# Kernel optimization log

Measured on AMD Instinct MI355X. Metric: run time of the kernel, lower is better.

Reference implementation:

```python
import jax, jax.numpy as jnp
import numpy as np

NUM_HEADS = 16  # concat repeats the identical head output this many times


def setup_inputs() -> dict:
    key = jax.random.key(0)
    ks = jax.random.split(key, 6)
    B, S, E, D = 4, 4096, 1024, 64  # D = E // NUM_HEADS
    s_in = 1.0 / np.sqrt(E)
    return {
        "x": jax.random.normal(ks[0], (B, S, E), dtype=jnp.float32),
        "Wq": jax.random.normal(ks[1], (E, D), dtype=jnp.float32) * s_in,
        "bq": jnp.zeros((D,), dtype=jnp.float32),
        "Wk": jax.random.normal(ks[2], (E, D), dtype=jnp.float32) * s_in,
        "bk": jnp.zeros((D,), dtype=jnp.float32),
        "Wv": jax.random.normal(ks[3], (E, D), dtype=jnp.float32) * s_in,
        "bv": jnp.zeros((D,), dtype=jnp.float32),
        "Wo": jax.random.normal(ks[4], (E, E), dtype=jnp.float32) * s_in,
        "bo": jnp.zeros((E,), dtype=jnp.float32),
    }


def reference(x, Wq, bq, Wk, bk, Wv, bv, Wo, bo):
    # Single shared projection to head_dim (the torch code projects E -> E//H once).
    q = x @ Wq + bq          # [B,S,D]
    k = x @ Wk + bk          # [B,S,D]
    v = x @ Wv + bv          # [B,S,D]
    d = q.shape[-1]
    scale = 1.0 / jnp.sqrt(jnp.asarray(d, dtype=q.dtype))
    scores = jnp.einsum("bqd,bkd->bqk", q, k) * scale   # [B,S,S]
    attn = jax.nn.softmax(scores, axis=-1)
    ctx = jnp.einsum("bqk,bkd->bqd", attn, v)            # [B,S,D]
    # Every head computes the identical result; concat == tile along features.
    cat = jnp.tile(ctx, (1, 1, NUM_HEADS))               # [B,S,E]
    return cat @ Wo + bo
```

## Files before the change

kernel.cpp:

```cpp
#include <hip/hip_runtime.h>
#include <hip/hip_bf16.h>

#define BB 4
#define SS 4096
#define EE 1024
#define DD 64

typedef unsigned short u16;
typedef unsigned int   u32;
typedef __bf16 bf16_t;
typedef bf16_t bf16x8 __attribute__((ext_vector_type(8)));
typedef float  f32x4  __attribute__((ext_vector_type(4)));
typedef u32    u32x4  __attribute__((ext_vector_type(4)));

__device__ __forceinline__ u16 f2bf(float f) {
    u32 u; __builtin_memcpy(&u, &f, 4);
    u32 r = (u + 0x7FFFu + ((u >> 16) & 1u)) >> 16;
    return (u16)r;
}
__device__ __forceinline__ u16 f2bf_fast(float f) {
    u32 u; __builtin_memcpy(&u, &f, 4);
    return (u16)((u + 0x8000u) >> 16);
}

__global__ __launch_bounds__(256) void wt_kernel(const float* __restrict__ Wq,
                                                 const float* __restrict__ Wk,
                                                 const float* __restrict__ Wv,
                                                 u16* __restrict__ Wt) {
    int t = blockIdx.x * 256 + threadIdx.x;
    int c = t >> 10, e = t & 1023;
    const float* W = (c < 64) ? Wq : (c < 128) ? Wk : Wv;
    Wt[c * 1024 + e] = f2bf(W[e * 64 + (c & 63)]);
}

__global__ __launch_bounds__(256) void wosum_kernel(const float* __restrict__ Wo,
                                                    float* __restrict__ WoSum) {
    int t = blockIdx.x * 256 + threadIdx.x;
    int d = t >> 10, e = t & 1023;
    float s = 0.f;
    #pragma unroll
    for (int h = 0; h < 16; h++) s += Wo[(h * 64 + d) * 1024 + e];
    WoSum[t] = s;
}

__global__ __launch_bounds__(256) void proj_kernel(const float* __restrict__ x,
                                                   const u16* __restrict__ Wtg,
                                                   const float* __restrict__ bq,
                                                   const float* __restrict__ bk,
                                                   const float* __restrict__ bv,
                                                   u16* __restrict__ Qg,
                                                   u16* __restrict__ Kg,
                                                   u16* __restrict__ Vtg) {
    __shared__ __align__(16) u16 xt[32 * 136];
    __shared__ __align__(16) u16 wts[192 * 136];

    const int tid  = threadIdx.x;
    const int w    = tid >> 6;
    const int lane = tid & 63;
    const int m    = lane & 15;
    const int quad = lane >> 4;
    const int r0   = blockIdx.x * 32;
    const int mt   = w & 1;
    const int ch   = w >> 1;

    f32x4 acc[6];
    #pragma unroll
    for (int i = 0; i < 6; i++) acc[i] = (f32x4){0.f, 0.f, 0.f, 0.f};

    f32x4 xr[4];
    u32x4 wr[12];

    auto preload = [&](int kb) {
        #pragma unroll
        for (int j = 0; j < 2; j++) {
            const int id = tid + j * 256, row = id >> 4, seg = id & 15;
            const float* src = x + (r0 + row) * 1024 + kb * 128 + seg * 8;
            xr[2 * j]     = *(const f32x4*)(src);
            xr[2 * j + 1] = *(const f32x4*)(src + 4);
        }
        #pragma unroll
        for (int j = 0; j < 12; j++) {
            const int id = tid + j * 256, row = id >> 4, seg = id & 15;
            wr[j] = *(const u32x4*)(Wtg + row * 1024 + kb * 128 + seg * 8);
        }
    };
    auto commit = [&]() {
        #pragma unroll
        for (int j = 0; j < 2; j++) {
            const int id = tid + j * 256, row = id >> 4, seg = id & 15;
            u32x4 p;
            p[0] = (u32)f2bf(xr[2*j][0])   | ((u32)f2bf(xr[2*j][1]) << 16);
            p[1] = (u32)f2bf(xr[2*j][2])   | ((u32)f2bf(xr[2*j][3]) << 16);
            p[2] = (u32)f2bf(xr[2*j+1][0]) | ((u32)f2bf(xr[2*j+1][1]) << 16);
            p[3] = (u32)f2bf(xr[2*j+1][2]) | ((u32)f2bf(xr[2*j+1][3]) << 16);
            *(u32x4*)(xt + row * 136 + seg * 8) = p;
        }
        #pragma unroll
        for (int j = 0; j < 12; j++) {
            const int id = tid + j * 256, row = id >> 4, seg = id & 15;
            *(u32x4*)(wts + row * 136 + seg * 8) = wr[j];
        }
    };

    preload(0);
    for (int kb = 0; kb < 8; kb++) {
        __syncthreads();
        commit();
        __syncthreads();
        if (kb < 7) preload(kb + 1);
        #pragma unroll
        for (int ks = 0; ks < 4; ks++) {
            bf16x8 a = *(const bf16x8*)(xt + (mt * 16 + m) * 136 + ks * 32 + quad * 8);
            #pragma unroll
            for (int c = 0; c < 6; c++) {
                bf16x8 b = *(const bf16x8*)(wts + (ch * 96 + c * 16 + m) * 136 + ks * 32 + quad * 8);
                acc[c] = __builtin_amdgcn_mfma_f32_16x16x32_bf16(a, b, acc[c], 0, 0, 0);
            }
        }
    }

    const int rbase = r0 + mt * 16 + quad * 4;
    #pragma unroll
    for (int c = 0; c < 6; c++) {
        const int col   = ch * 96 + c * 16 + m;
        const int which = col >> 6;
        const int d     = col & 63;
        const float bias = (which == 0 ? bq : which == 1 ? bk : bv)[d];
        #pragma unroll
        for (int r = 0; r < 4; r++) {
            const int row = rbase + r;
            float v = acc[c][r] + bias;
            if (which == 0) {
                Qg[row * 64 + d] = f2bf(v * 0.125f);
            } else if (which == 1) {
                Kg[row * 64 + d] = f2bf(v);
            } else {
                const int b = row >> 12, s = row & 4095;
                Vtg[(b * 64 + d) * 4096 + s] = f2bf(v);
            }
        }
    }
}

#define ATTN_LDS 147456
__global__ __launch_bounds__(512) void attn_kernel(const u16* __restrict__ Qg,
                                                   const u16* __restrict__ Kg,
                                                   const u16* __restrict__ Vtg,
                                                   float* __restrict__ ctxg) {
    extern __shared__ __align__(16) u16 smem[];

    const int tid  = threadIdx.x;
    const int w    = tid >> 6;
    const int lane = tid & 63;
    const int m    = lane & 15;
    const int quad = lane >> 4;

    const int bi    = blockIdx.x;
    const int batch = (bi >> 1) & 3;
    const int qt    = ((bi >> 3) << 1) | (bi & 1);
    const int qrow0 = batch * 4096 + qt * 64;

    u16* wbase = smem + w * 9216;

    bf16x8 aq[4][2];
    #pragma unroll
    for (int s = 0; s < 4; s++) {
        aq[s][0] = *(const bf16x8*)(Qg + (qrow0 + s * 16 + m) * 64 + quad * 8);
        aq[s][1] = *(const bf16x8*)(Qg + (qrow0 + s * 16 + m) * 64 + 32 + quad * 8);
    }

    f32x4 acc[4][4];
    float li[4][4];
    #pragma unroll
    for (int s = 0; s < 4; s++)
        #pragma unroll
        for (int c = 0; c < 4; c++) {
            acc[s][c] = (f32x4){0.f, 0.f, 0.f, 0.f};
            li[s][c] = 0.f;
        }

    const u16* Kbase = Kg + batch * 4096 * 64;
    const u16* Vbase = Vtg + batch * 64 * 4096;

    const int rl8 = lane >> 3, sg8 = lane & 7;
    const int rv  = lane >> 2, sv  = lane & 3;

    u32x4 kr[4], vr[4];
    auto preload = [&](int it) {
        const int k0 = (w + it * 8) * 32;
        #pragma unroll
        for (int i = 0; i < 4; i++) {
            kr[i] = *(const u32x4*)(Kbase + (k0 + rl8 + 8 * i) * 64 + sg8 * 8);
            vr[i] = *(const u32x4*)(Vbase + (rv + 16 * i) * 4096 + k0 + sv * 8);
        }
    };
    auto commitKV = [&](int p) {
        u16* Kt = wbase + p * 4608;
        u16* Vt = Kt + 2560;
        #pragma unroll
        for (int i = 0; i < 4; i++) {
            *(u32x4*)(Kt + (rl8 + 8 * i) * 64 + ((sg8 ^ rl8) * 8)) = kr[i];
            *(u32x4*)(Vt + (rv + 16 * i) * 32 + sv * 8) = vr[i];
        }
    };

    const float LOG2E = 1.4426950408889634f;
    const float NC2   = -12.0f * 1.4426950408889634f;

    preload(0);
    commitKV(0);

    for (int it = 0; it < 16; it++) {
        const int pcur = it & 1;
        u16* Kt = wbase + pcur * 4608;
        u16* Vt = Kt + 2560;
        u16* P  = Kt;

        if (it < 15) preload(it + 1);

        f32x4 sc[4][2];
        #pragma unroll
        for (int c = 0; c < 2; c++) {
            const int key = c * 16 + m;
            bf16x8 b0 = *(const bf16x8*)(Kt + key * 64 + ((quad ^ (m & 7)) * 8));
            bf16x8 b1 = *(const bf16x8*)(Kt + key * 64 + (((quad | 4) ^ (m & 7)) * 8));
            #pragma unroll
            for (int s = 0; s < 4; s++) {
                f32x4 t = __builtin_amdgcn_mfma_f32_16x16x32_bf16(aq[s][0], b0, (f32x4){0.f,0.f,0.f,0.f}, 0, 0, 0);
                sc[s][c] = __builtin_amdgcn_mfma_f32_16x16x32_bf16(aq[s][1], b1, t, 0, 0, 0);
            }
        }

        #pragma unroll
        for (int s = 0; s < 4; s++) {
            #pragma unroll
            for (int r = 0; r < 4; r++) {
                const float p0 = __builtin_exp2f(__builtin_fmaf(sc[s][0][r], LOG2E, NC2));
                const float p1 = __builtin_exp2f(__builtin_fmaf(sc[s][1][r], LOG2E, NC2));
                li[s][r] += p0 + p1;
                const int row = s * 16 + quad * 4 + r;
                P[row * 40 + m]      = f2bf_fast(p0);
                P[row * 40 + 16 + m] = f2bf_fast(p1);
            }
        }

        bf16x8 ap[4];
        #pragma unroll
        for (int s = 0; s < 4; s++)
            ap[s] = *(const bf16x8*)(P + (s * 16 + m) * 40 + quad * 8);
        #pragma unroll
        for (int c = 0; c < 4; c++) {
            bf16x8 bv = *(const bf16x8*)(Vt + (c * 16 + m) * 32 + quad * 8);
            #pragma unroll
            for (int s = 0; s < 4; s++)
                acc[s][c] = __builtin_amdgcn_mfma_f32_16x16x32_bf16(ap[s], bv, acc[s][c], 0, 0, 0);
        }

        if (it < 15) commitKV((it + 1) & 1);
    }

    #pragma unroll
    for (int s = 0; s < 4; s++)
        #pragma unroll
        for (int r = 0; r < 4; r++) {
            float v = li[s][r];
            v += __shfl_xor(v, 1);
            v += __shfl_xor(v, 2);
            v += __shfl_xor(v, 4);
            v += __shfl_xor(v, 8);
            li[s][r] = v;
        }

    __syncthreads();
    float* mf = (float*)smem;
    if (w >= 4) {
        float* cb = mf + (w - 4) * 4160;
        #pragma unroll
        for (int s = 0; s < 4; s++)
            #pragma unroll
            for (int c = 0; c < 4; c++)
                #pragma unroll
                for (int r = 0; r < 4; r++)
                    cb[(s * 16 + quad * 4 + r) * 64 + c * 16 + m] = acc[s][c][r];
        if (m == 0) {
            #pragma unroll
            for (int s = 0; s < 4; s++)
                #pragma unroll
                for (int r = 0; r < 4; r++)
                    cb[4096 + s * 16 + quad * 4 + r] = li[s][r];
        }
    }
    __syncthreads();
    if (w < 4) {
        float* cb = mf + w * 4160;
        #pragma unroll
        for (int s = 0; s < 4; s++)
            #pragma unroll
            for (int c = 0; c < 4; c++)
                #pragma unroll
                for (int r = 0; r < 4; r++)
                    acc[s][c][r] += cb[(s * 16 + quad * 4 + r) * 64 + c * 16 + m];
        #pragma unroll
        for (int s = 0; s < 4; s++)
            #pragma unroll
            for (int r = 0; r < 4; r++)
                li[s][r] += cb[4096 + s * 16 + quad * 4 + r];
        #pragma unroll
        for (int s = 0; s < 4; s++)
            #pragma unroll
            for (int c = 0; c < 4; c++)
                #pragma unroll
                for (int r = 0; r < 4; r++)
                    cb[(s * 16 + quad * 4 + r) * 64 + c * 16 + m] = acc[s][c][r];
        if (m == 0) {
            #pragma unroll
            for (int s = 0; s < 4; s++)
                #pragma unroll
                for (int r = 0; r < 4; r++)
                    cb[4096 + s * 16 + quad * 4 + r] = li[s][r];
        }
    }
    __syncthreads();

    const int q  = tid >> 3;
    const int d0 = (tid & 7) * 8;
    float L = 0.f;
    f32x4 o0 = (f32x4){0.f, 0.f, 0.f, 0.f};
    f32x4 o1 = (f32x4){0.f, 0.f, 0.f, 0.f};
    #pragma unroll
    for (int j = 0; j < 4; j++) {
        const float* cb = mf + j * 4160;
        L  += cb[4096 + q];
        o0 += *(const f32x4*)(cb + q * 64 + d0);
        o1 += *(const f32x4*)(cb + q * 64 + d0 + 4);
    }
    const float inv = 1.0f / L;
    o0 *= inv; o1 *= inv;
    *(f32x4*)(ctxg + (qrow0 + q) * 64 + d0)     = o0;
    *(f32x4*)(ctxg + (qrow0 + q) * 64 + d0 + 4) = o1;
}

__global__ __launch_bounds__(256) void out_kernel(const float* __restrict__ ctxg,
                                                  const float* __restrict__ WoSum,
                                                  const float* __restrict__ bo,
                                                  float* __restrict__ out) {
    __shared__ float cl[64 * 64];
    const int tid = threadIdx.x;
    const int r0  = (blockIdx.x >> 2) * 64;
    const int eb  = (blockIdx.x & 3) * 256;

    #pragma unroll
    for (int j = 0; j < 4; j++) {
        const int pos = (tid + j * 256) * 4;
        *(f32x4*)(cl + pos) = *(const f32x4*)(ctxg + r0 * 64 + pos);
    }
    __syncthreads();

    const int rg = tid >> 6;
    const int cg = tid & 63;
    const int e0 = eb + cg * 4;

    f32x4 bo4 = *(const f32x4*)(bo + e0);
    f32x4 a[16];
    #pragma unroll
    for (int r = 0; r < 16; r++) a[r] = bo4;

    for (int d = 0; d < 64; d++) {
        f32x4 wv = *(const f32x4*)(WoSum + d * 1024 + e0);
        #pragma unroll
        for (int r = 0; r < 16; r++) {
            a[r] += wv * cl[(rg * 16 + r) * 64 + d];
        }
    }
    #pragma unroll
    for (int r = 0; r < 16; r++) {
        *(f32x4*)(out + (r0 + rg * 16 + r) * 1024 + e0) = a[r];
    }
}

extern "C" void kernel_launch(void* const* d_in, const int* in_sizes, int n_in,
                              void* d_out, int out_size, void* d_ws, size_t ws_size,
                              hipStream_t stream) {
    const float* x  = (const float*)d_in[0];
    const float* Wq = (const float*)d_in[1];
    const float* bq = (const float*)d_in[2];
    const float* Wk = (const float*)d_in[3];
    const float* bk = (const float*)d_in[4];
    const float* Wv = (const float*)d_in[5];
    const float* bv = (const float*)d_in[6];
    const float* Wo = (const float*)d_in[7];
    const float* bo = (const float*)d_in[8];
    float* out = (float*)d_out;

    char* ws = (char*)d_ws;
    u16*   Wt   = (u16*)(ws);
    float* WoS  = (float*)(ws + 393216);
    u16*   Qg   = (u16*)(ws + 655360);
    u16*   Kg   = (u16*)(ws + 2752512);
    u16*   Vtg  = (u16*)(ws + 4849664);
    float* ctxg = (float*)(ws + 6946816);

    (void)hipFuncSetAttribute((const void*)attn_kernel,
                              hipFuncAttributeMaxDynamicSharedMemorySize, ATTN_LDS);

    wt_kernel   <<<768,  256, 0, stream>>>(Wq, Wk, Wv, Wt);
    wosum_kernel<<<256,  256, 0, stream>>>(Wo, WoS);
    proj_kernel <<<512,  256, 0, stream>>>(x, Wt, bq, bk, bv, Qg, Kg, Vtg);
    attn_kernel <<<256,  512, ATTN_LDS, stream>>>(Qg, Kg, Vtg, ctxg);
    out_kernel  <<<1024, 256, 0, stream>>>(ctxg, WoS, bo, out);
}
```

Before: 217.5 us.

## Split attention keys across two blocks, merge partials in output kernel

The attention kernel now splits each batch's keys into two halves handled by separate blocks, doubling the grid to 512 blocks. It drops the LDS double buffer to halve shared memory and adds a launch-bounds occupancy hint. Each block writes unnormalized partial context and row sums, and the output GEMM kernel adds the two halves and applies the 1/L normalization. The kernel also computes row sums with an MFMA against a ones vector instead of shuffles, uses hardware bf16 conversion and packed P stores with a permuted V layout, and pads the reduction scratch to cut bank conflicts. This is meant to raise occupancy and parallelism on the 256-CU device, at the cost of extra partial-result traffic and a single-buffered K/V pipeline.

```diff
diff --git a/kernel.cpp b/kernel.cpp
--- a/kernel.cpp
+++ b/kernel.cpp
@@ -9,18 +9,15 @@
 typedef unsigned short u16;
 typedef unsigned int   u32;
 typedef __bf16 bf16_t;
+typedef bf16_t bf16x2 __attribute__((ext_vector_type(2)));
 typedef bf16_t bf16x8 __attribute__((ext_vector_type(8)));
 typedef float  f32x4  __attribute__((ext_vector_type(4)));
 typedef u32    u32x4  __attribute__((ext_vector_type(4)));
 
-__device__ __forceinline__ u16 f2bf(float f) {
-    u32 u; __builtin_memcpy(&u, &f, 4);
-    u32 r = (u + 0x7FFFu + ((u >> 16) & 1u)) >> 16;
-    return (u16)r;
-}
-__device__ __forceinline__ u16 f2bf_fast(float f) {
-    u32 u; __builtin_memcpy(&u, &f, 4);
-    return (u16)((u + 0x8000u) >> 16);
+__device__ __forceinline__ u16 f2bf_hw(float f) {
+    bf16_t b = (bf16_t)f;
+    u16 u; __builtin_memcpy(&u, &b, 2);
+    return u;
 }
 
 __global__ __launch_bounds__(256) void wt_kernel(const float* __restrict__ Wq,
@@ -30,7 +27,7 @@
     int t = blockIdx.x * 256 + threadIdx.x;
     int c = t >> 10, e = t & 1023;
     const float* W = (c < 64) ? Wq : (c < 128) ? Wk : Wv;
-    Wt[c * 1024 + e] = f2bf(W[e * 64 + (c & 63)]);
+    Wt[c * 1024 + e] = f2bf_hw(W[e * 64 + (c & 63)]);
 }
 
 __global__ __launch_bounds__(256) void wosum_kernel(const float* __restrict__ Wo,
@@ -88,12 +85,13 @@
         #pragma unroll
         for (int j = 0; j < 2; j++) {
             const int id = tid + j * 256, row = id >> 4, seg = id & 15;
-            u32x4 p;
-            p[0] = (u32)f2bf(xr[2*j][0])   | ((u32)f2bf(xr[2*j][1]) << 16);
-            p[1] = (u32)f2bf(xr[2*j][2])   | ((u32)f2bf(xr[2*j][3]) << 16);
-            p[2] = (u32)f2bf(xr[2*j+1][0]) | ((u32)f2bf(xr[2*j+1][1]) << 16);
-            p[3] = (u32)f2bf(xr[2*j+1][2]) | ((u32)f2bf(xr[2*j+1][3]) << 16);
-            *(u32x4*)(xt + row * 136 + seg * 8) = p;
+            bf16x8 v;
+            #pragma unroll
+            for (int k = 0; k < 4; k++) {
+                v[k]     = (bf16_t)xr[2 * j][k];
+                v[4 + k] = (bf16_t)xr[2 * j + 1][k];
+            }
+            *(bf16x8*)(xt + row * 136 + seg * 8) = v;
         }
         #pragma unroll
         for (int j = 0; j < 12; j++) {
@@ -131,22 +129,24 @@
             const int row = rbase + r;
             float v = acc[c][r] + bias;
             if (which == 0) {
-                Qg[row * 64 + d] = f2bf(v * 0.125f);
+                Qg[row * 64 + d] = f2bf_hw(v * 0.125f);
             } else if (which == 1) {
-                Kg[row * 64 + d] = f2bf(v);
+                Kg[row * 64 + d] = f2bf_hw(v);
             } else {
                 const int b = row >> 12, s = row & 4095;
-                Vtg[(b * 64 + d) * 4096 + s] = f2bf(v);
+                const int sp = (s & ~31) | (((s & 15) << 1) | ((s >> 4) & 1));
+                Vtg[(b * 64 + d) * 4096 + sp] = f2bf_hw(v);
             }
         }
     }
 }
 
-#define ATTN_LDS 147456
-__global__ __launch_bounds__(512) void attn_kernel(const u16* __restrict__ Qg,
-                                                   const u16* __restrict__ Kg,
-                                                   const u16* __restrict__ Vtg,
-                                                   float* __restrict__ ctxg) {
+#define ATTN_LDS 73728
+__global__ __launch_bounds__(512, 4) void attn_kernel(const u16* __restrict__ Qg,
+                                                      const u16* __restrict__ Kg,
+                                                      const u16* __restrict__ Vtg,
+                                                      float* __restrict__ ctxP,
+                                                      float* __restrict__ liP) {
     extern __shared__ __align__(16) u16 smem[];
 
     const int tid  = threadIdx.x;
@@ -156,11 +156,14 @@
     const int quad = lane >> 4;
 
     const int bi    = blockIdx.x;
+    const int khalf = bi & 1;
     const int batch = (bi >> 1) & 3;
-    const int qt    = ((bi >> 3) << 1) | (bi & 1);
+    const int qt    = bi >> 3;
     const int qrow0 = batch * 4096 + qt * 64;
 
-    u16* wbase = smem + w * 9216;
+    u16* wbase = smem + w * 4608;
+    u16* Kt = wbase;
+    u16* Vt = wbase + 2560;
 
     bf16x8 aq[4][2];
     #pragma unroll
@@ -170,17 +173,20 @@
     }
 
     f32x4 acc[4][4];
-    float li[4][4];
-    #pragma unroll
-    for (int s = 0; s < 4; s++)
-        #pragma unroll
-        for (int c = 0; c < 4; c++) {
-            acc[s][c] = (f32x4){0.f, 0.f, 0.f, 0.f};
-            li[s][c] = 0.f;
-        }
-
-    const u16* Kbase = Kg + batch * 4096 * 64;
-    const u16* Vbase = Vtg + batch * 64 * 4096;
+    f32x4 accli[4];
+    #pragma unroll
+    for (int s = 0; s < 4; s++) {
+        accli[s] = (f32x4){0.f, 0.f, 0.f, 0.f};
+        #pragma unroll
+        for (int c = 0; c < 4; c++) acc[s][c] = (f32x4){0.f, 0.f, 0.f, 0.f};
+    }
+
+    bf16x8 ones;
+    #pragma unroll
+    for (int k = 0; k < 8; k++) ones[k] = (bf16_t)1.0f;
+
+    const u16* Kbase = Kg + (batch * 4096 + khalf * 2048) * 64;
+    const u16* Vbase = Vtg + batch * 64 * 4096 + khalf * 2048;
 
     const int rl8 = lane >> 3, sg8 = lane & 7;
     const int rv  = lane >> 2, sv  = lane & 3;
@@ -194,9 +200,7 @@
             vr[i] = *(const u32x4*)(Vbase + (rv + 16 * i) * 4096 + k0 + sv * 8);
         }
     };
-    auto commitKV = [&](int p) {
-        u16* Kt = wbase + p * 4608;
-        u16* Vt = Kt + 2560;
+    auto commitKV = [&]() {
         #pragma unroll
         for (int i = 0; i < 4; i++) {
             *(u32x4*)(Kt + (rl8 + 8 * i) * 64 + ((sg8 ^ rl8) * 8)) = kr[i];
@@ -208,15 +212,10 @@
     const float NC2   = -12.0f * 1.4426950408889634f;
 
     preload(0);
-    commitKV(0);
-
-    for (int it = 0; it < 16; it++) {
-        const int pcur = it & 1;
-        u16* Kt = wbase + pcur * 4608;
-        u16* Vt = Kt + 2560;
-        u16* P  = Kt;
-
-        if (it < 15) preload(it + 1);
+    commitKV();
+
+    for (int it = 0; it < 8; it++) {
+        if (it < 7) preload(it + 1);
 
         f32x4 sc[4][2];
         #pragma unroll
@@ -231,16 +230,19 @@
             }
         }
 
+        u16* P = Kt;
         #pragma unroll
         for (int s = 0; s < 4; s++) {
             #pragma unroll
             for (int r = 0; r < 4; r++) {
                 const float p0 = __builtin_exp2f(__builtin_fmaf(sc[s][0][r], LOG2E, NC2));
                 const float p1 = __builtin_exp2f(__builtin_fmaf(sc[s][1][r], LOG2E, NC2));
-                li[s][r] += p0 + p1;
                 const int row = s * 16 + quad * 4 + r;
-                P[row * 40 + m]      = f2bf_fast(p0);
-                P[row * 40 + 16 + m] = f2bf_fast(p1);
+                bf16x2 pr;
+                pr[0] = (bf16_t)p0;
+                pr[1] = (bf16_t)p1;
+                u32 pu; __builtin_memcpy(&pu, &pr, 4);
+                *(u32*)(P + row * 40 + 2 * m) = pu;
             }
         }
 
@@ -248,6 +250,9 @@
         #pragma unroll
         for (int s = 0; s < 4; s++)
             ap[s] = *(const bf16x8*)(P + (s * 16 + m) * 40 + quad * 8);
+        #pragma unroll
+        for (int s = 0; s < 4; s++)
+            accli[s] = __builtin_amdgcn_mfma_f32_16x16x32_bf16(ap[s], ones, accli[s], 0, 0, 0);
         #pragma unroll
         for (int c = 0; c < 4; c++) {
             bf16x8 bv = *(const bf16x8*)(Vt + (c * 16 + m) * 32 + quad * 8);
@@ -256,68 +261,59 @@
                 acc[s][c] = __builtin_amdgcn_mfma_f32_16x16x32_bf16(ap[s], bv, acc[s][c], 0, 0, 0);
         }
 
-        if (it < 15) commitKV((it + 1) & 1);
-    }
-
-    #pragma unroll
-    for (int s = 0; s < 4; s++)
-        #pragma unroll
-        for (int r = 0; r < 4; r++) {
-            float v = li[s][r];
-            v += __shfl_xor(v, 1);
-            v += __shfl_xor(v, 2);
-            v += __shfl_xor(v, 4);
-            v += __shfl_xor(v, 8);
-            li[s][r] = v;
-        }
+        if (it < 7) {
+            asm volatile("s_waitcnt lgkmcnt(0)" ::: "memory");
+            commitKV();
+        }
+    }
 
     __syncthreads();
     float* mf = (float*)smem;
     if (w >= 4) {
-        float* cb = mf + (w - 4) * 4160;
+        float* cb = mf + (w - 4) * 4416;
         #pragma unroll
         for (int s = 0; s < 4; s++)
             #pragma unroll
             for (int c = 0; c < 4; c++)
                 #pragma unroll
                 for (int r = 0; r < 4; r++)
-                    cb[(s * 16 + quad * 4 + r) * 64 + c * 16 + m] = acc[s][c][r];
+                    cb[(s * 16 + quad * 4 + r) * 68 + c * 16 + m] = acc[s][c][r];
         if (m == 0) {
             #pragma unroll
             for (int s = 0; s < 4; s++)
                 #pragma unroll
                 for (int r = 0; r < 4; r++)
-                    cb[4096 + s * 16 + quad * 4 + r] = li[s][r];
+                    cb[4352 + s * 16 + quad * 4 + r] = accli[s][r];
         }
     }
     __syncthreads();
     if (w < 4) {
-        float* cb = mf + w * 4160;
+        float* cb = mf + w * 4416;
         #pragma unroll
         for (int s = 0; s < 4; s++)
             #pragma unroll
             for (int c = 0; c < 4; c++)
                 #pragma unroll
                 for (int r = 0; r < 4; r++)
-                    acc[s][c][r] += cb[(s * 16 + quad * 4 + r) * 64 + c * 16 + m];
+                    acc[s][c][r] += cb[(s * 16 + quad * 4 + r) * 68 + c * 16 + m];
         #pragma unroll
         for (int s = 0; s < 4; s++)
             #pragma unroll
             for (int r = 0; r < 4; r++)
-                li[s][r] += cb[4096 + s * 16 + quad * 4 + r];
+                accli[s][r] += cb[4352 + s * 16 + quad * 4 + r];
         #pragma unroll
         for (int s = 0; s < 4; s++)
             #pragma unroll
             for (int c = 0; c < 4; c++)
                 #pragma unroll
                 for (int r = 0; r < 4; r++)
-                    cb[(s * 16 + quad * 4 + r) * 64 + c * 16 + m] = acc[s][c][r];
+                    cb[(s * 16 + quad * 4 + r) * 68 + c * 16 + m] = acc[s][c][r];
         if (m == 0) {
             #pragma unroll
             for (int s = 0; s < 4; s++)
                 #pragma unroll
                 for (int r = 0; r < 4; r++)
-                    cb[4096 + s * 16 + quad * 4 + r] = li[s][r];
+                    cb[4352 + s * 16 + quad * 4 + r] = accli[s][r];
         }
     }
     __syncthreads();
@@ -329,30 +325,39 @@
     f32x4 o1 = (f32x4){0.f, 0.f, 0.f, 0.f};
     #pragma unroll
     for (int j = 0; j < 4; j++) {
-        const float* cb = mf + j * 4160;
-        L  += cb[4096 + q];
-        o0 += *(const f32x4*)(cb + q * 64 + d0);
-        o1 += *(const f32x4*)(cb + q * 64 + d0 + 4);
-    }
-    const float inv = 1.0f / L;
-    o0 *= inv; o1 *= inv;
-    *(f32x4*)(ctxg + (qrow0 + q) * 64 + d0)     = o0;
-    *(f32x4*)(ctxg + (qrow0 + q) * 64 + d0 + 4) = o1;
-}
-
-__global__ __launch_bounds__(256) void out_kernel(const float* __restrict__ ctxg,
+        const float* cb = mf + j * 4416;
+        L  += cb[4352 + q];
+        o0 += *(const f32x4*)(cb + q * 68 + d0);
+        o1 += *(const f32x4*)(cb + q * 68 + d0 + 4);
+    }
+    const int gr = khalf * 16384 + qrow0 + q;
+    *(f32x4*)(ctxP + gr * 64 + d0)     = o0;
+    *(f32x4*)(ctxP + gr * 64 + d0 + 4) = o1;
+    if ((tid & 7) == 0) liP[gr] = L;
+}
+
+__global__ __launch_bounds__(256) void out_kernel(const float* __restrict__ ctxP,
+                                                  const float* __restrict__ liP,
                                                   const float* __restrict__ WoSum,
                                                   const float* __restrict__ bo,
                                                   float* __restrict__ out) {
     __shared__ float cl[64 * 64];
+    __shared__ float linv[64];
     const int tid = threadIdx.x;
     const int r0  = (blockIdx.x >> 2) * 64;
     const int eb  = (blockIdx.x & 3) * 256;
 
+    if (tid < 64) {
+        linv[tid] = 1.0f / (liP[r0 + tid] + liP[16384 + r0 + tid]);
+    }
+    const float* A = ctxP + r0 * 64;
+    const float* B = ctxP + 16384 * 64 + r0 * 64;
     #pragma unroll
     for (int j = 0; j < 4; j++) {
         const int pos = (tid + j * 256) * 4;
-        *(f32x4*)(cl + pos) = *(const f32x4*)(ctxg + r0 * 64 + pos);
+        f32x4 a4 = *(const f32x4*)(A + pos);
+        f32x4 b4 = *(const f32x4*)(B + pos);
+        *(f32x4*)(cl + pos) = a4 + b4;
     }
     __syncthreads();
 
@@ -360,10 +365,9 @@
     const int cg = tid & 63;
     const int e0 = eb + cg * 4;
 
-    f32x4 bo4 = *(const f32x4*)(bo + e0);
     f32x4 a[16];
     #pragma unroll
-    for (int r = 0; r < 16; r++) a[r] = bo4;
+    for (int r = 0; r < 16; r++) a[r] = (f32x4){0.f, 0.f, 0.f, 0.f};
 
     for (int d = 0; d < 64; d++) {
         f32x4 wv = *(const f32x4*)(WoSum + d * 1024 + e0);
@@ -372,9 +376,11 @@
             a[r] += wv * cl[(rg * 16 + r) * 64 + d];
         }
     }
+    f32x4 bo4 = *(const f32x4*)(bo + e0);
     #pragma unroll
     for (int r = 0; r < 16; r++) {
-        *(f32x4*)(out + (r0 + rg * 16 + r) * 1024 + e0) = a[r];
+        f32x4 o = a[r] * linv[rg * 16 + r] + bo4;
+        *(f32x4*)(out + (r0 + rg * 16 + r) * 1024 + e0) = o;
     }
 }
 
@@ -398,7 +404,8 @@
     u16*   Qg   = (u16*)(ws + 655360);
     u16*   Kg   = (u16*)(ws + 2752512);
     u16*   Vtg  = (u16*)(ws + 4849664);
-    float* ctxg = (float*)(ws + 6946816);
+    float* ctxP = (float*)(ws + 6946816);
+    float* liP  = (float*)(ws + 15335424);
 
     (void)hipFuncSetAttribute((const void*)attn_kernel,
                               hipFuncAttributeMaxDynamicSharedMemorySize, ATTN_LDS);
@@ -406,6 +413,6 @@
     wt_kernel   <<<768,  256, 0, stream>>>(Wq, Wk, Wv, Wt);
     wosum_kernel<<<256,  256, 0, stream>>>(Wo, WoS);
     proj_kernel <<<512,  256, 0, stream>>>(x, Wt, bq, bk, bv, Qg, Kg, Vtg);
-    attn_kernel <<<256,  512, ATTN_LDS, stream>>>(Qg, Kg, Vtg, ctxg);
-    out_kernel  <<<1024, 256, 0, stream>>>(ctxg, WoS, bo, out);
-}
+    attn_kernel <<<512,  512, ATTN_LDS, stream>>>(Qg, Kg, Vtg, ctxP, liP);
+    out_kernel  <<<1024, 256, 0, stream>>>(ctxP, liP, WoS, bo, out);
+}
```

Measured after the change: 312.3 us. +43.6%, slower.
